# Performance work log

Hardware: AMD Instinct MI355X
Metric: run time of the kernel (lower is better)

The kernel has to match this reference:

```python
import jax, jax.numpy as jnp
import numpy as np

N_NODES = 50000
N_EDGES = 1600000
IN_DIM = 128
HID = 128


def setup_inputs() -> dict:
    key = jax.random.key(0)
    ks = jax.random.split(key, 12)
    s = 1.0 / np.sqrt(HID)
    return {
        "x": jax.random.normal(ks[0], (N_NODES, IN_DIM), jnp.float32),
        "src": jax.random.randint(ks[1], (N_EDGES,), 0, N_NODES, jnp.int32),
        "dst": jax.random.randint(ks[2], (N_EDGES,), 0, N_NODES, jnp.int32),
        "W0": jax.random.normal(ks[3], (IN_DIM, HID), jnp.float32) * s,
        "b0": jnp.zeros((HID,), jnp.float32),
        "W1": jax.random.normal(ks[4], (HID, HID), jnp.float32) * s,
        "b1": jnp.zeros((HID,), jnp.float32),
        "W2": jax.random.normal(ks[5], (HID, HID), jnp.float32) * s,
        "b2": jnp.zeros((HID,), jnp.float32),
        "w_pg": jax.random.normal(ks[6], (HID, 1), jnp.float32) * s,
        "b_pg": jnp.zeros((1,), jnp.float32),
        "w_pd": jax.random.normal(ks[7], (HID, 1), jnp.float32) * s,
        "b_pd": jnp.zeros((1,), jnp.float32),
        "w_v": jax.random.normal(ks[8], (HID, 1), jnp.float32) * s,
        "b_v": jnp.zeros((1,), jnp.float32),
    }


def _gcn_layer(h, src, dst, W, b):
    # DGL-style GCN: gather source features along edges, sum-scatter to dst,
    # then per-node Linear + ReLU.  agg: [N, d]
    agg = jax.ops.segment_sum(h[src], dst, num_segments=N_NODES)
    return jax.nn.relu(agg @ W + b)


def reference(x, src, dst, W0, b0, W1, b1, W2, b2, w_pg, b_pg, w_pd, b_pd, w_v, b_v):
    h = _gcn_layer(x, src, dst, W0, b0)
    h = _gcn_layer(h, src, dst, W1, b1)
    h = _gcn_layer(h, src, dst, W2, b2)
    mN = jnp.mean(h, axis=0, keepdims=True)          # dgl.mean_nodes -> [1, HID]
    v = mN @ w_v + b_v                                # [1, 1]
    pi_graph = h @ w_pg + b_pg                        # [N, 1]
    pi_done = mN @ w_pd + b_pd                        # [1, 1]
    pi = jnp.concatenate([pi_graph, pi_done], axis=0)  # [N+1, 1]
    return (pi, v)
```

## Files before the change

kernel.cpp:

```cpp
#include <hip/hip_runtime.h>
#include <hip/hip_bf16.h>


#define HID 128
#define NBLK 256
#define BSH 6
#define SCAN_CHUNK 1024

typedef __attribute__((ext_vector_type(8))) short short8;
typedef __attribute__((ext_vector_type(4))) float f32x4;

__device__ __forceinline__ unsigned int f2bf(float f) {
    unsigned int u = __float_as_uint(f);
    return (u + 0x7fffu + ((u >> 16) & 1u)) >> 16;
}

__global__ __launch_bounds__(256) void f32_to_bf16_kernel(
        const float4* __restrict__ in, ushort4* __restrict__ out, int n4) {
    for (int i = blockIdx.x * blockDim.x + threadIdx.x; i < n4; i += gridDim.x * blockDim.x) {
        float4 v = in[i];
        ushort4 o;
        o.x = (unsigned short)f2bf(v.x); o.y = (unsigned short)f2bf(v.y);
        o.z = (unsigned short)f2bf(v.z); o.w = (unsigned short)f2bf(v.w);
        out[i] = o;
    }
}

__global__ __launch_bounds__(256) void pack_w3_kernel(
        const float* __restrict__ W0, const float* __restrict__ W1,
        const float* __restrict__ W2, unsigned short* __restrict__ pw) {
    for (int j = blockIdx.x * blockDim.x + threadIdx.x; j < 3 * 16384;
         j += gridDim.x * blockDim.x) {
        int jj = j & 16383, which = j >> 14;
        const float* W = (which == 0) ? W0 : (which == 1) ? W1 : W2;
        int i = jj & 7, lane = (jj >> 3) & 63, kk = (jj >> 9) & 3, c = (jj >> 11) & 7;
        int k = kk * 32 + (lane >> 4) * 8 + i;
        int col = c * 16 + (lane & 15);
        pw[j] = (unsigned short)f2bf(W[k * 128 + col]);
    }
}

__global__ __launch_bounds__(256) void bhist_kernel(const int* __restrict__ dst,
        int* __restrict__ tbl, int ne, int nb, int epb) {
    __shared__ int lcnt[1024];
    const int k = blockIdx.x, t = threadIdx.x;
    for (int b = t; b < nb; b += 256) lcnt[b] = 0;
    __syncthreads();
    const int beg = k * epb, end = min(ne, beg + epb);
    for (int j = beg + t; j < end; j += 256)
        atomicAdd(&lcnt[dst[j] >> BSH], 1);
    __syncthreads();
    for (int b = t; b < nb; b += 256) tbl[b * NBLK + k] = lcnt[b];
}

__global__ __launch_bounds__(256) void scan_p1_kernel(const int* __restrict__ tbl,
        int* __restrict__ bsum, int sz) {
    __shared__ int sh[256];
    const int g = blockIdx.x, t = threadIdx.x;
    const int base = g * SCAN_CHUNK + t * 4;
    int s = 0;
    if (base + 3 < sz) {
        int4 v = *(const int4*)(tbl + base);
        s = v.x + v.y + v.z + v.w;
    } else {
        for (int i = 0; i < 4; ++i) if (base + i < sz) s += tbl[base + i];
    }
    sh[t] = s;
    __syncthreads();
    for (int off = 128; off > 0; off >>= 1) {
        if (t < off) sh[t] += sh[t + off];
        __syncthreads();
    }
    if (t == 0) bsum[g] = sh[0];
}

__global__ __launch_bounds__(256) void scan_p2_kernel(int* __restrict__ bsum, int ng) {
    __shared__ int sh[256];
    const int t = threadIdx.x;
    int v = (t < ng) ? bsum[t] : 0;
    sh[t] = v;
    __syncthreads();
    for (int off = 1; off < 256; off <<= 1) {
        int a = sh[t];
        int b = (t >= off) ? sh[t - off] : 0;
        __syncthreads();
        sh[t] = a + b;
        __syncthreads();
    }
    if (t < ng) bsum[t] = sh[t] - v;
}

__global__ __launch_bounds__(256) void scan_p3_kernel(int* __restrict__ tbl,
        const int* __restrict__ bsum, int sz) {
    __shared__ int sh[256];
    const int g = blockIdx.x, t = threadIdx.x;
    const int base = g * SCAN_CHUNK + t * 4;
    int4 v = make_int4(0, 0, 0, 0);
    if (base + 3 < sz) {
        v = *(const int4*)(tbl + base);
    } else {
        if (base + 0 < sz) v.x = tbl[base + 0];
        if (base + 1 < sz) v.y = tbl[base + 1];
        if (base + 2 < sz) v.z = tbl[base + 2];
    }
    int s = v.x + v.y + v.z + v.w;
    sh[t] = s;
    __syncthreads();
    for (int off = 1; off < 256; off <<= 1) {
        int a = sh[t];
        int b = (t >= off) ? sh[t - off] : 0;
        __syncthreads();
        sh[t] = a + b;
        __syncthreads();
    }
    int pre = bsum[g] + sh[t] - s;
    int o0 = pre, o1 = pre + v.x, o2 = o1 + v.y, o3 = o2 + v.z;
    if (base + 3 < sz) {
        *(int4*)(tbl + base) = make_int4(o0, o1, o2, o3);
    } else {
        if (base + 0 < sz) tbl[base + 0] = o0;
        if (base + 1 < sz) tbl[base + 1] = o1;
        if (base + 2 < sz) tbl[base + 2] = o2;
    }
}

__global__ __launch_bounds__(256) void bucket_scatter_kernel(
        const int* __restrict__ src, const int* __restrict__ dst,
        const int* __restrict__ tbl, int* __restrict__ pairs,
        int ne, int nb, int epb) {
    __shared__ int cur[1024];
    const int k = blockIdx.x, t = threadIdx.x;
    for (int b = t; b < nb; b += 256) cur[b] = tbl[b * NBLK + k];
    __syncthreads();
    const int beg = k * epb, end = min(ne, beg + epb);
    for (int j = beg + t; j < end; j += 256) {
        int d = dst[j];
        int pos = atomicAdd(&cur[d >> BSH], 1);
        pairs[pos] = (src[j] << BSH) | (d & 63);
    }
}

__global__ __launch_bounds__(256) void fine_scatter_kernel(
        const int* __restrict__ pairs, const int* __restrict__ tbl,
        int* __restrict__ row_ptr, int* __restrict__ eidx,
        int ne, int nb, int n) {
    __shared__ int cnt[64], cur[64];
    const int b = blockIdx.x, t = threadIdx.x;
    const int node0 = b << BSH;
    if (t < 64) cnt[t] = 0;
    __syncthreads();
    const int beg = tbl[b * NBLK];
    const int end = (b == nb - 1) ? ne : tbl[(b + 1) * NBLK];
    for (int j = beg + t; j < end; j += 256) atomicAdd(&cnt[pairs[j] & 63], 1);
    __syncthreads();
    if (t == 0) {
        int run = beg;
        #pragma unroll
        for (int i = 0; i < 64; ++i) { cur[i] = run; run += cnt[i]; }
    }
    __syncthreads();
    if (t < 64 && node0 + t < n) row_ptr[node0 + t] = cur[t];
    if (b == nb - 1 && t == 0) row_ptr[n] = ne;
    __syncthreads();
    for (int j = beg + t; j < end; j += 256) {
        int v = pairs[j];
        int pos = atomicAdd(&cur[v & 63], 1);
        eidx[pos] = v >> BSH;
    }
}

#define ACC8(V)  {                                                        \
    acc[0] += __uint_as_float((V).x << 16);                               \
    acc[1] += __uint_as_float((V).x & 0xffff0000u);                       \
    acc[2] += __uint_as_float((V).y << 16);                               \
    acc[3] += __uint_as_float((V).y & 0xffff0000u);                       \
    acc[4] += __uint_as_float((V).z << 16);                               \
    acc[5] += __uint_as_float((V).z & 0xffff0000u);                       \
    acc[6] += __uint_as_float((V).w << 16);                               \
    acc[7] += __uint_as_float((V).w & 0xffff0000u); }

__global__ __launch_bounds__(256) void aggregate_bf_kernel(
        const uint4* __restrict__ xb, const int* __restrict__ row_ptr,
        const int* __restrict__ eidx, uint4* __restrict__ aggb, int n) {
    int g = (int)((blockIdx.x * blockDim.x + threadIdx.x) >> 5);
    int lane = threadIdx.x & 31;
    if (g >= n) return;
    const int half = lane >> 4, l16 = lane & 15;
    const int beg = row_ptr[g], end = row_ptr[g + 1];
    float acc[8] = {};
    int e = beg;
    for (; e + 16 <= end; e += 16) {
        uint4 v0 = xb[(size_t)eidx[e + 0 + half] * 16 + l16];
        uint4 v1 = xb[(size_t)eidx[e + 2 + half] * 16 + l16];
        uint4 v2 = xb[(size_t)eidx[e + 4 + half] * 16 + l16];
        uint4 v3 = xb[(size_t)eidx[e + 6 + half] * 16 + l16];
        uint4 v4 = xb[(size_t)eidx[e + 8 + half] * 16 + l16];
        uint4 v5 = xb[(size_t)eidx[e + 10 + half] * 16 + l16];
        uint4 v6 = xb[(size_t)eidx[e + 12 + half] * 16 + l16];
        uint4 v7 = xb[(size_t)eidx[e + 14 + half] * 16 + l16];
        ACC8(v0); ACC8(v1); ACC8(v2); ACC8(v3);
        ACC8(v4); ACC8(v5); ACC8(v6); ACC8(v7);
    }
    for (; e + 4 <= end; e += 4) {
        uint4 v0 = xb[(size_t)eidx[e + 0 + half] * 16 + l16];
        uint4 v1 = xb[(size_t)eidx[e + 2 + half] * 16 + l16];
        ACC8(v0); ACC8(v1);
    }
    for (; e < end; e += 2) {
        int idx = e + half;
        uint4 v = make_uint4(0, 0, 0, 0);
        if (idx < end) v = xb[(size_t)eidx[idx] * 16 + l16];
        ACC8(v);
    }
    #pragma unroll
    for (int j = 0; j < 8; ++j) acc[j] += __shfl_xor(acc[j], 16);
    if (half == 0) {
        uint4 o;
        o.x = f2bf(acc[0]) | (f2bf(acc[1]) << 16);
        o.y = f2bf(acc[2]) | (f2bf(acc[3]) << 16);
        o.z = f2bf(acc[4]) | (f2bf(acc[5]) << 16);
        o.w = f2bf(acc[6]) | (f2bf(acc[7]) << 16);
        aggb[(size_t)g * 16 + l16] = o;
    }
}

__global__ __launch_bounds__(256) void gemm_mfma_kernel(
        const short* __restrict__ A, const short* __restrict__ packw,
        const float* __restrict__ bias, unsigned short* __restrict__ out, int M,
        float* __restrict__ part, float* __restrict__ pig_out,
        const float* __restrict__ w_pg, const float* __restrict__ b_pg) {
    __shared__ float colp[4][128];
    const int w = threadIdx.x >> 6, l = threadIdx.x & 63;
    const int m = l & 15, hi = l >> 4;
    const int row0 = blockIdx.x * 64 + w * 16;
    const int arow = row0 + m;
    const bool valid = arow < M;

    short8 afrag[4];
    #pragma unroll
    for (int kk = 0; kk < 4; ++kk) {
        if (valid)
            afrag[kk] = *(const short8*)(A + (size_t)arow * 128 + kk * 32 + hi * 8);
        else
            afrag[kk] = short8{0, 0, 0, 0, 0, 0, 0, 0};
    }

    f32x4 acc[8] = {};
    #pragma unroll
    for (int kk = 0; kk < 4; ++kk) {
        #pragma unroll
        for (int c = 0; c < 8; ++c) {
            short8 bfrag = *(const short8*)(packw + ((size_t)(c * 4 + kk) * 64 + l) * 8);
            acc[c] = __builtin_amdgcn_mfma_f32_16x16x32_bf16(afrag[kk], bfrag, acc[c], 0, 0, 0);
        }
    }

    float hvv[8][4];
    #pragma unroll
    for (int c = 0; c < 8; ++c) {
        float bcol = bias[c * 16 + m];
        #pragma unroll
        for (int r = 0; r < 4; ++r) {
            int row = row0 + hi * 4 + r;
            float hv = (row < M) ? fmaxf(acc[c][r] + bcol, 0.f) : 0.f;
            hvv[c][r] = hv;
            if (row < M)
                out[(size_t)row * 128 + c * 16 + m] = (unsigned short)f2bf(hv);
        }
    }

    if (w_pg) {
        #pragma unroll
        for (int r = 0; r < 4; ++r) {
            float p = 0.f;
            #pragma unroll
            for (int c = 0; c < 8; ++c) p += hvv[c][r] * w_pg[c * 16 + m];
            #pragma unroll
            for (int off = 1; off < 16; off <<= 1) p += __shfl_xor(p, off);
            int row = row0 + hi * 4 + r;
            if (m == 0 && row < M) pig_out[row] = p + b_pg[0];
        }
        #pragma unroll
        for (int c = 0; c < 8; ++c) {
            float v = hvv[c][0] + hvv[c][1] + hvv[c][2] + hvv[c][3];
            v += __shfl_xor(v, 16);
            v += __shfl_xor(v, 32);
            if (hi == 0) colp[w][c * 16 + m] = v;
        }
        __syncthreads();
        const int t = threadIdx.x;
        if (t < 128)
            part[(size_t)blockIdx.x * 128 + t] =
                colp[0][t] + colp[1][t] + colp[2][t] + colp[3][t];
    }
}

__global__ __launch_bounds__(1024) void head_final_kernel(
        const float* __restrict__ part, int nparts,
        const float* __restrict__ w_v, const float* __restrict__ b_v,
        const float* __restrict__ w_pd, const float* __restrict__ b_pd,
        float* __restrict__ out, int n_nodes) {
    __shared__ float sh[32][128];
    __shared__ float sv[128], sd[128];
    const int t = threadIdx.x;
    const int d4 = t & 31, pg = t >> 5;
    float4 acc = make_float4(0.f, 0.f, 0.f, 0.f);
    for (int i = pg; i < nparts; i += 32) {
        float4 v = *(const float4*)(part + (size_t)i * 128 + d4 * 4);
        acc.x += v.x; acc.y += v.y; acc.z += v.z; acc.w += v.w;
    }
    *(float4*)&sh[pg][d4 * 4] = acc;
    __syncthreads();
    for (int off = 16; off > 0; off >>= 1) {
        if (pg < off) {
            float4 a = *(float4*)&sh[pg][d4 * 4];
            float4 b = *(float4*)&sh[pg + off][d4 * 4];
            a.x += b.x; a.y += b.y; a.z += b.z; a.w += b.w;
            *(float4*)&sh[pg][d4 * 4] = a;
        }
        __syncthreads();
    }
    if (t < 128) {
        float mm = sh[0][t] / (float)n_nodes;
        sv[t] = mm * w_v[t];
        sd[t] = mm * w_pd[t];
    }
    __syncthreads();
    for (int off = 64; off > 0; off >>= 1) {
        if (t < off) { sv[t] += sv[t + off]; sd[t] += sd[t + off]; }
        __syncthreads();
    }
    if (t == 0) {
        out[n_nodes] = sd[0] + b_pd[0];
        out[n_nodes + 1] = sv[0] + b_v[0];
    }
}

static inline size_t align_up(size_t v, size_t a) { return (v + a - 1) & ~(a - 1); }

extern "C" void kernel_launch(void* const* d_in, const int* in_sizes, int n_in,
                              void* d_out, int out_size, void* d_ws, size_t ws_size,
                              hipStream_t stream) {
    const float* x    = (const float*)d_in[0];
    const int*   src  = (const int*)d_in[1];
    const int*   dst  = (const int*)d_in[2];
    const float* W0   = (const float*)d_in[3];
    const float* b0   = (const float*)d_in[4];
    const float* W1   = (const float*)d_in[5];
    const float* b1   = (const float*)d_in[6];
    const float* W2   = (const float*)d_in[7];
    const float* b2   = (const float*)d_in[8];
    const float* w_pg = (const float*)d_in[9];
    const float* b_pg = (const float*)d_in[10];
    const float* w_pd = (const float*)d_in[11];
    const float* b_pd = (const float*)d_in[12];
    const float* w_v  = (const float*)d_in[13];
    const float* b_v  = (const float*)d_in[14];
    float* out = (float*)d_out;

    const int NN = in_sizes[0] / HID;
    const int NE = in_sizes[1];
    const int NB = (NN + 63) >> BSH;
    const int SZ = NB * NBLK;
    const int EPB = (NE + NBLK - 1) / NBLK;
    const int NG = (SZ + SCAN_CHUNK - 1) / SCAN_CHUNK;
    const int GBLK = (NN + 63) / 64;

    char* w = (char*)d_ws;
    int* tbl      = (int*)w;            w += align_up((size_t)SZ * 4, 256);
    int* bsum     = (int*)w;            w += align_up((size_t)256 * 4, 256);
    int* row_ptr  = (int*)w;            w += align_up((size_t)(NN + 1) * 4, 256);
    int* eidx     = (int*)w;            w += align_up((size_t)NE * 4, 256);
    unsigned short* xb   = (unsigned short*)w; w += align_up((size_t)NN * HID * 2, 256);
    unsigned short* aggb = (unsigned short*)w; w += align_up((size_t)NN * HID * 2, 256);
    unsigned short* hb   = (unsigned short*)w; w += align_up((size_t)NN * HID * 2, 256);
    unsigned short* pw   = (unsigned short*)w; w += align_up((size_t)3 * 16384 * 2, 256);
    float* part   = (float*)w;          w += align_up((size_t)GBLK * 128 * 4, 256);
    int* pairs    = (int*)aggb;
    (void)ws_size; (void)n_in; (void)out_size;

    f32_to_bf16_kernel<<<2048, 256, 0, stream>>>((const float4*)x, (ushort4*)xb, NN * 32);
    pack_w3_kernel<<<48, 256, 0, stream>>>(W0, W1, W2, pw);

    bhist_kernel<<<NBLK, 256, 0, stream>>>(dst, tbl, NE, NB, EPB);
    scan_p1_kernel<<<NG, 256, 0, stream>>>(tbl, bsum, SZ);
    scan_p2_kernel<<<1, 256, 0, stream>>>(bsum, NG);
    scan_p3_kernel<<<NG, 256, 0, stream>>>(tbl, bsum, SZ);
    bucket_scatter_kernel<<<NBLK, 256, 0, stream>>>(src, dst, tbl, pairs, NE, NB, EPB);
    fine_scatter_kernel<<<NB, 256, 0, stream>>>(pairs, tbl, row_ptr, eidx, NE, NB, NN);

    const int agg_blocks = (NN * 32 + 255) / 256;

    aggregate_bf_kernel<<<agg_blocks, 256, 0, stream>>>((const uint4*)xb, row_ptr, eidx,
                                                        (uint4*)aggb, NN);
    gemm_mfma_kernel<<<GBLK, 256, 0, stream>>>((const short*)aggb, (const short*)pw,
                                               b0, hb, NN, nullptr, nullptr, nullptr, nullptr);
    aggregate_bf_kernel<<<agg_blocks, 256, 0, stream>>>((const uint4*)hb, row_ptr, eidx,
                                                        (uint4*)aggb, NN);
    gemm_mfma_kernel<<<GBLK, 256, 0, stream>>>((const short*)aggb, (const short*)(pw + 16384),
                                               b1, hb, NN, nullptr, nullptr, nullptr, nullptr);
    aggregate_bf_kernel<<<agg_blocks, 256, 0, stream>>>((const uint4*)hb, row_ptr, eidx,
                                                        (uint4*)aggb, NN);
    gemm_mfma_kernel<<<GBLK, 256, 0, stream>>>((const short*)aggb, (const short*)(pw + 32768),
                                               b2, hb, NN, part, out, w_pg, b_pg);

    head_final_kernel<<<1, 1024, 0, stream>>>(part, GBLK, w_v, b_v, w_pd, b_pd, out, NN);
}
```

Before: 265.8 us.

## Compute per-node degrees in histogram pass, vectorize edge loads, pack bf16 accumulation

The bucket histogram kernel now also counts per-node in-degrees with global atomics into a degree array that is zeroed inside the weight-packing kernel. This lets the fine scatter kernel skip its own counting pass over the pairs. The histogram and bucket scatter kernels read dst and src as int4, with the per-block edge count rounded to a multiple of four. The aggregation kernel accumulates into float2 vectors, which may allow packed FP32 adds. The trade-off is 1.6M extra global atomics, contended on the same node counters, in exchange for removing one LDS-atomic pass.

```diff
diff --git a/kernel.cpp b/kernel.cpp
--- a/kernel.cpp
+++ b/kernel.cpp
@@ -9,10 +9,16 @@
 
 typedef __attribute__((ext_vector_type(8))) short short8;
 typedef __attribute__((ext_vector_type(4))) float f32x4;
+typedef __attribute__((ext_vector_type(2))) float f32x2;
+typedef __attribute__((ext_vector_type(2))) unsigned int u32x2;
 
 __device__ __forceinline__ unsigned int f2bf(float f) {
     unsigned int u = __float_as_uint(f);
     return (u + 0x7fffu + ((u >> 16) & 1u)) >> 16;
+}
+__device__ __forceinline__ f32x2 bfpair(unsigned int u) {
+    u32x2 t = {u << 16, u & 0xffff0000u};
+    return __builtin_bit_cast(f32x2, t);
 }
 
 __global__ __launch_bounds__(256) void f32_to_bf16_kernel(
@@ -28,9 +34,11 @@
 
 __global__ __launch_bounds__(256) void pack_w3_kernel(
         const float* __restrict__ W0, const float* __restrict__ W1,
-        const float* __restrict__ W2, unsigned short* __restrict__ pw) {
-    for (int j = blockIdx.x * blockDim.x + threadIdx.x; j < 3 * 16384;
-         j += gridDim.x * blockDim.x) {
+        const float* __restrict__ W2, unsigned short* __restrict__ pw,
+        int4* __restrict__ deg4, int n4z) {
+    int z = blockIdx.x * blockDim.x + threadIdx.x;
+    if (z < n4z) deg4[z] = make_int4(0, 0, 0, 0);
+    for (int j = z; j < 3 * 16384; j += gridDim.x * blockDim.x) {
         int jj = j & 16383, which = j >> 14;
         const float* W = (which == 0) ? W0 : (which == 1) ? W1 : W2;
         int i = jj & 7, lane = (jj >> 3) & 63, kk = (jj >> 9) & 3, c = (jj >> 11) & 7;
@@ -41,14 +49,24 @@
 }
 
 __global__ __launch_bounds__(256) void bhist_kernel(const int* __restrict__ dst,
-        int* __restrict__ tbl, int ne, int nb, int epb) {
+        int* __restrict__ tbl, int* __restrict__ deg, int ne, int nb, int epb) {
     __shared__ int lcnt[1024];
     const int k = blockIdx.x, t = threadIdx.x;
     for (int b = t; b < nb; b += 256) lcnt[b] = 0;
     __syncthreads();
     const int beg = k * epb, end = min(ne, beg + epb);
-    for (int j = beg + t; j < end; j += 256)
-        atomicAdd(&lcnt[dst[j] >> BSH], 1);
+    int j = beg + t * 4;
+    for (; j + 3 < end; j += 1024) {
+        int4 d = *(const int4*)(dst + j);
+        atomicAdd(&lcnt[d.x >> BSH], 1); atomicAdd(&deg[d.x], 1);
+        atomicAdd(&lcnt[d.y >> BSH], 1); atomicAdd(&deg[d.y], 1);
+        atomicAdd(&lcnt[d.z >> BSH], 1); atomicAdd(&deg[d.z], 1);
+        atomicAdd(&lcnt[d.w >> BSH], 1); atomicAdd(&deg[d.w], 1);
+    }
+    for (; j < end; ++j) {
+        int d = dst[j];
+        atomicAdd(&lcnt[d >> BSH], 1); atomicAdd(&deg[d], 1);
+    }
     __syncthreads();
     for (int b = t; b < nb; b += 256) tbl[b * NBLK + k] = lcnt[b];
 }
@@ -133,7 +151,16 @@
     for (int b = t; b < nb; b += 256) cur[b] = tbl[b * NBLK + k];
     __syncthreads();
     const int beg = k * epb, end = min(ne, beg + epb);
-    for (int j = beg + t; j < end; j += 256) {
+    int j = beg + t * 4;
+    for (; j + 3 < end; j += 1024) {
+        int4 d = *(const int4*)(dst + j);
+        int4 s = *(const int4*)(src + j);
+        int p0 = atomicAdd(&cur[d.x >> BSH], 1); pairs[p0] = (s.x << BSH) | (d.x & 63);
+        int p1 = atomicAdd(&cur[d.y >> BSH], 1); pairs[p1] = (s.y << BSH) | (d.y & 63);
+        int p2 = atomicAdd(&cur[d.z >> BSH], 1); pairs[p2] = (s.z << BSH) | (d.z & 63);
+        int p3 = atomicAdd(&cur[d.w >> BSH], 1); pairs[p3] = (s.w << BSH) | (d.w & 63);
+    }
+    for (; j < end; ++j) {
         int d = dst[j];
         int pos = atomicAdd(&cur[d >> BSH], 1);
         pairs[pos] = (src[j] << BSH) | (d & 63);
@@ -142,21 +169,18 @@
 
 __global__ __launch_bounds__(256) void fine_scatter_kernel(
         const int* __restrict__ pairs, const int* __restrict__ tbl,
+        const int* __restrict__ deg,
         int* __restrict__ row_ptr, int* __restrict__ eidx,
         int ne, int nb, int n) {
-    __shared__ int cnt[64], cur[64];
+    __shared__ int cur[64];
     const int b = blockIdx.x, t = threadIdx.x;
     const int node0 = b << BSH;
-    if (t < 64) cnt[t] = 0;
-    __syncthreads();
     const int beg = tbl[b * NBLK];
     const int end = (b == nb - 1) ? ne : tbl[(b + 1) * NBLK];
-    for (int j = beg + t; j < end; j += 256) atomicAdd(&cnt[pairs[j] & 63], 1);
-    __syncthreads();
     if (t == 0) {
         int run = beg;
         #pragma unroll
-        for (int i = 0; i < 64; ++i) { cur[i] = run; run += cnt[i]; }
+        for (int i = 0; i < 64; ++i) { cur[i] = run; run += deg[node0 + i]; }
     }
     __syncthreads();
     if (t < 64 && node0 + t < n) row_ptr[node0 + t] = cur[t];
@@ -169,15 +193,8 @@
     }
 }
 
-#define ACC8(V)  {                                                        \
-    acc[0] += __uint_as_float((V).x << 16);                               \
-    acc[1] += __uint_as_float((V).x & 0xffff0000u);                       \
-    acc[2] += __uint_as_float((V).y << 16);                               \
-    acc[3] += __uint_as_float((V).y & 0xffff0000u);                       \
-    acc[4] += __uint_as_float((V).z << 16);                               \
-    acc[5] += __uint_as_float((V).z & 0xffff0000u);                       \
-    acc[6] += __uint_as_float((V).w << 16);                               \
-    acc[7] += __uint_as_float((V).w & 0xffff0000u); }
+#define ACC8(V)  { a01 += bfpair((V).x); a23 += bfpair((V).y);            \
+                   a45 += bfpair((V).z); a67 += bfpair((V).w); }
 
 __global__ __launch_bounds__(256) void aggregate_bf_kernel(
         const uint4* __restrict__ xb, const int* __restrict__ row_ptr,
@@ -187,7 +204,7 @@
     if (g >= n) return;
     const int half = lane >> 4, l16 = lane & 15;
     const int beg = row_ptr[g], end = row_ptr[g + 1];
-    float acc[8] = {};
+    f32x2 a01 = {0.f, 0.f}, a23 = {0.f, 0.f}, a45 = {0.f, 0.f}, a67 = {0.f, 0.f};
     int e = beg;
     for (; e + 16 <= end; e += 16) {
         uint4 v0 = xb[(size_t)eidx[e + 0 + half] * 16 + l16];
@@ -212,6 +229,7 @@
         if (idx < end) v = xb[(size_t)eidx[idx] * 16 + l16];
         ACC8(v);
     }
+    float acc[8] = {a01.x, a01.y, a23.x, a23.y, a45.x, a45.y, a67.x, a67.y};
     #pragma unroll
     for (int j = 0; j < 8; ++j) acc[j] += __shfl_xor(acc[j], 16);
     if (half == 0) {
@@ -362,13 +380,15 @@
     const int NE = in_sizes[1];
     const int NB = (NN + 63) >> BSH;
     const int SZ = NB * NBLK;
-    const int EPB = (NE + NBLK - 1) / NBLK;
+    const int EPB = (((NE + NBLK - 1) / NBLK) + 3) & ~3;
     const int NG = (SZ + SCAN_CHUNK - 1) / SCAN_CHUNK;
     const int GBLK = (NN + 63) / 64;
+    const int NDEG = NB * 64;
 
     char* w = (char*)d_ws;
     int* tbl      = (int*)w;            w += align_up((size_t)SZ * 4, 256);
     int* bsum     = (int*)w;            w += align_up((size_t)256 * 4, 256);
+    int* deg      = (int*)w;            w += align_up((size_t)NDEG * 4, 256);
     int* row_ptr  = (int*)w;            w += align_up((size_t)(NN + 1) * 4, 256);
     int* eidx     = (int*)w;            w += align_up((size_t)NE * 4, 256);
     unsigned short* xb   = (unsigned short*)w; w += align_up((size_t)NN * HID * 2, 256);
@@ -380,14 +400,14 @@
     (void)ws_size; (void)n_in; (void)out_size;
 
     f32_to_bf16_kernel<<<2048, 256, 0, stream>>>((const float4*)x, (ushort4*)xb, NN * 32);
-    pack_w3_kernel<<<48, 256, 0, stream>>>(W0, W1, W2, pw);
-
-    bhist_kernel<<<NBLK, 256, 0, stream>>>(dst, tbl, NE, NB, EPB);
+    pack_w3_kernel<<<64, 256, 0, stream>>>(W0, W1, W2, pw, (int4*)deg, NDEG / 4);
+
+    bhist_kernel<<<NBLK, 256, 0, stream>>>(dst, tbl, deg, NE, NB, EPB);
     scan_p1_kernel<<<NG, 256, 0, stream>>>(tbl, bsum, SZ);
     scan_p2_kernel<<<1, 256, 0, stream>>>(bsum, NG);
     scan_p3_kernel<<<NG, 256, 0, stream>>>(tbl, bsum, SZ);
     bucket_scatter_kernel<<<NBLK, 256, 0, stream>>>(src, dst, tbl, pairs, NE, NB, EPB);
-    fine_scatter_kernel<<<NB, 256, 0, stream>>>(pairs, tbl, row_ptr, eidx, NE, NB, NN);
+    fine_scatter_kernel<<<NB, 256, 0, stream>>>(pairs, tbl, deg, row_ptr, eidx, NE, NB, NN);
 
     const int agg_blocks = (NN * 32 + 255) / 256;
 
```

New measurement: 321.8 us. +21.1%, slower.
